# Kernel optimization log

Hardware: AMD Instinct MI355X
Metric: run time of the kernel (lower is better)

The kernel has to match this reference:

```python
import jax, jax.numpy as jnp
import numpy as np

V = 64                 # |Sigma|
IN_DIM = V + 2         # Sigma + '(' + ')'
OUT_DIM = V + 1        # Sigma + <del>/<end>
H = 512
B = 256
SX = 34                # max proto length 32 + 2 boundaries
SY = 34
BIG_NEG = -1000000000.0


def _one_hot_seq(key, S, batch):
    # '(' at pos 0, L random symbols, ')' at pos L+1, zero padding after
    kl, ks = jax.random.split(key)
    lengths = jax.random.randint(kl, (batch,), 4, S - 1)        # L in [4, S-2]
    syms = jax.random.randint(ks, (S, batch), 0, V)
    pos = jnp.arange(S)[:, None]
    tok = jnp.where(pos == 0, V, jnp.where(pos == lengths[None, :] + 1, V + 1, syms))
    oh = jax.nn.one_hot(tok, IN_DIM, dtype=jnp.float32)
    valid = (pos <= lengths[None, :] + 1).astype(jnp.float32)
    return oh * valid[:, :, None]


def setup_inputs() -> dict:
    key = jax.random.key(0)
    ks = jax.random.split(key, 14)

    def p(k, shape, scale):
        return jax.random.uniform(k, shape, jnp.float32, -scale, scale)

    s = 1.0 / float(np.sqrt(H))
    s2 = 1.0 / float(np.sqrt(2 * H))
    return {
        "sources": _one_hot_seq(ks[0], SX, B),
        "targets": _one_hot_seq(ks[1], SY, B),
        # bidirectional prior LSTM (input IN_DIM -> hidden H, fwd + rev)
        "Wih_f": p(ks[2], (4 * H, IN_DIM), s), "Whh_f": p(ks[3], (4 * H, H), s), "b_f": p(ks[4], (4 * H,), s),
        "Wih_r": p(ks[5], (4 * H, IN_DIM), s), "Whh_r": p(ks[6], (4 * H, H), s), "b_r": p(ks[7], (4 * H,), s),
        # modern LSTM (input IN_DIM -> hidden 2H)
        "Wih_m": p(ks[8], (8 * H, IN_DIM), s2), "Whh_m": p(ks[9], (8 * H, 2 * H), s2), "b_m": p(ks[10], (8 * H,), s2),
        # heads: Linear(2H -> OUT_DIM) + LogSoftmax
        "W_sub": p(ks[11], (OUT_DIM, 2 * H), s2), "b_sub": jnp.zeros((OUT_DIM,), jnp.float32),
        "W_ins": p(ks[12], (OUT_DIM, 2 * H), s2), "b_ins": jnp.zeros((OUT_DIM,), jnp.float32),
    }


def _lstm(x, Wih, Whh, b, hid):
    # torch gate order: i, f, g, o
    bsz = x.shape[1]
    def step(carry, xt):
        h, c = carry
        g = xt @ Wih.T + h @ Whh.T + b
        i, f, gg, o = jnp.split(g, 4, axis=-1)
        c = jax.nn.sigmoid(f) * c + jax.nn.sigmoid(i) * jnp.tanh(gg)
        h = jax.nn.sigmoid(o) * jnp.tanh(c)
        return (h, c), h
    init = (jnp.zeros((bsz, hid), x.dtype), jnp.zeros((bsz, hid), x.dtype))
    _, hs = jax.lax.scan(step, init, x)
    return hs  # [S, B, hid]


def _forward(sources, targets, Wih_f, Whh_f, b_f, Wih_r, Whh_r, b_r,
             Wih_m, Whh_m, b_m, W_sub, b_sub, W_ins, b_ins):
    x_fwd = _lstm(sources, Wih_f, Whh_f, b_f, H)
    x_bwd = _lstm(sources[::-1], Wih_r, Whh_r, b_r, H)[::-1]
    x_emb = jnp.concatenate([x_fwd, x_bwd], axis=-1)   # [SX, B, 2H]
    y_emb = _lstm(targets, Wih_m, Whh_m, b_m, 2 * H)    # [SY, B, 2H]

    # head(x_emb[i] + y_emb[j]) decomposes since Linear is affine
    def pair_logprobs(W, bb):
        lx = jnp.einsum('ibh,oh->ibo', x_emb, W)              # [SX, B, O]
        ly = jnp.einsum('jbh,oh->jbo', y_emb, W) + bb         # [SY, B, O]
        return jax.nn.log_softmax(lx[:, None] + ly[None, :], axis=-1)  # [SX, SY, B, O]

    sub_log = pair_logprobs(W_sub, b_sub)
    ins_log = pair_logprobs(W_ins, b_ins)

    # cell (i, j, b) is computed iff x[i] and y[j] are real (non-padding) one-hots, j <= max_cognat_length
    x_any = sources.sum(-1) > 0                                # [SX, B]
    y_any = targets.sum(-1) > 0                                # [SY, B]
    j_ok = jnp.arange(SY) < SY - 1
    valid = x_any[:, None, :] & (y_any & j_ok[:, None])[None, :, :]   # [SX, SY, B]

    end = jnp.where(valid, ins_log[..., V], BIG_NEG)           # insProbs[V_SIZE]
    dlt = jnp.where(valid, sub_log[..., V], BIG_NEG)           # subProbs[V_SIZE]

    y_next = jnp.pad(targets[1:], ((0, 1), (0, 0), (0, 0)))    # y[j+1], [SY, B, IN_DIM]
    ins_ok = valid & (y_next[..., IN_DIM - 1] == 0)[None]      # not bool(y[j+1, V_SIZE+1])
    ins_val = jnp.einsum('ijbv,jbv->ijb', ins_log[..., :V], y_next[..., :V])
    sub_val = jnp.einsum('ijbv,jbv->ijb', sub_log[..., :V], y_next[..., :V])

    # stacked cached probs: [ins, sub, end, del], each [SX, SY, B]
    return jnp.stack([
        jnp.where(ins_ok, ins_val, BIG_NEG),
        jnp.where(ins_ok, sub_val, BIG_NEG),
        end,
        dlt,
    ])


def reference(sources, targets, Wih_f, Whh_f, b_f, Wih_r, Whh_r, b_r,
              Wih_m, Whh_m, b_m, W_sub, b_sub, W_ins, b_ins):
    return _forward(sources, targets, Wih_f, Whh_f, b_f, Wih_r, Whh_r, b_r,
                    Wih_m, Whh_m, b_m, W_sub, b_sub, W_ins, b_ins)
```

## Files before the change

kernel.cpp:

```cpp
#include <hip/hip_runtime.h>

typedef __attribute__((ext_vector_type(4))) float f32x4;
typedef unsigned char u8;
typedef unsigned long long u64t;

#define BIG_NEG -1000000000.0f

static constexpr int B_  = 256;
static constexpr int SX_ = 34;
static constexpr int SY_ = 34;
static constexpr int IND = 66;
static constexpr int OP_ = 80;

__device__ __forceinline__ f32x4 mfma_fp8(long a, long b, f32x4 c) {
  return __builtin_amdgcn_mfma_f32_16x16x32_fp8_fp8(a, b, c, 0, 0, 0);
}
__device__ __forceinline__ float sigm(float x)  { return 1.0f / (1.0f + __expf(-x)); }
__device__ __forceinline__ float tanhx(float x) { return 2.0f * sigm(2.0f * x) - 1.0f; }
template <bool HI>
__device__ __forceinline__ unsigned pk2(float a, float b, unsigned old) {
  return __builtin_amdgcn_cvt_pk_fp8_f32(a, b, (int)old, HI);
}

__global__ __launch_bounds__(256) void prep_all(
    const float* __restrict__ src, const float* __restrict__ tgt,
    int* __restrict__ tok_x, int* __restrict__ tok_y,
    const float* __restrict__ Wsub, const float* __restrict__ Wins,
    u8* __restrict__ Wcat,
    const float* __restrict__ Wihf, const float* __restrict__ bf,
    const float* __restrict__ Wihr, const float* __restrict__ br,
    const float* __restrict__ Wihm, const float* __restrict__ bm,
    float* __restrict__ Ef, float* __restrict__ Er, float* __restrict__ Em,
    const float* __restrict__ Whf, const float* __restrict__ Whr,
    const float* __restrict__ Whm,
    u8* __restrict__ w8f, u8* __restrict__ w8r, u8* __restrict__ w8m) {
  __shared__ float tile[64 * 67];
  const int blk = blockIdx.x;
  const int tid = threadIdx.x;

  if (blk < 68) {
    int idx = blk * 256 + tid;
    const int half = SX_ * B_;
    const float* base = (idx < half) ? src : tgt;
    int* outp         = (idx < half) ? tok_x : tok_y;
    int k = (idx < half) ? idx : idx - half;
    const float* p = base + (size_t)k * IND;
    int tok = -1;
    for (int v = 0; v < IND; ++v) if (p[v] > 0.5f) tok = v;
    outp[k] = tok;
  } else if (blk < 228) {
    int widx = (blk - 68) * 256 + tid;
    int row = widx >> 8;
    int wc  = widx & 255;
    int srow = row < 80 ? row : row - 80;
    const float* W = row < 80 ? Wsub : Wins;
    float f0 = 0.f, f1 = 0.f, f2 = 0.f, f3 = 0.f;
    if (srow < 65) {
      const float* p = W + (size_t)srow * 1024 + wc * 4;
      f0 = p[0]; f1 = p[1]; f2 = p[2]; f3 = p[3];
    }
    unsigned w = pk2<false>(f0, f1, 0);
    w = pk2<true>(f2, f3, w);
    ((unsigned*)Wcat)[widx] = w;
  } else if (blk < 356) {
    int tb = blk - 228;
    const float* W; const float* bias; float* E; int H4; int n0;
    if (tb < 32)      { W = Wihf; bias = bf; E = Ef; H4 = 2048; n0 = tb * 64; }
    else if (tb < 64) { W = Wihr; bias = br; E = Er; H4 = 2048; n0 = (tb - 32) * 64; }
    else              { W = Wihm; bias = bm; E = Em; H4 = 4096; n0 = (tb - 64) * 64; }
    const float* s2 = W + (size_t)n0 * IND;
    for (int i = tid; i < 64 * IND; i += 256) {
      int n = i / IND, v = i - n * IND;
      tile[n * 67 + v] = s2[i];
    }
    __syncthreads();
    int lane = tid & 63, w2 = tid >> 6;
    float bl = bias[n0 + lane];
    for (int v = w2; v < 67; v += 4) {
      float val = (v < 66 ? tile[lane * 67 + v] : 0.f) + bl;
      E[(size_t)v * H4 + n0 + lane] = val;
    }
  } else {
    const int F4 = 2048 * 512 / 4;
    const int M4 = 4096 * 1024 / 4;
    int i = (blk - 356) * 256 + tid;
    int stride = 3072 * 256;
    for (; i < 2 * F4 + M4; i += stride) {
      const float* s3; unsigned* dst; int k;
      if (i < F4)          { s3 = Whf; dst = (unsigned*)w8f; k = i; }
      else if (i < 2 * F4) { s3 = Whr; dst = (unsigned*)w8r; k = i - F4; }
      else                 { s3 = Whm; dst = (unsigned*)w8m; k = i - 2 * F4; }
      float4 f = ((const float4*)s3)[k];
      unsigned w3 = pk2<false>(f.x, f.y, 0);
      w3 = pk2<true>(f.z, f.w, w3);
      dst[k] = w3;
    }
  }
}

template <int HH>
__device__ __forceinline__ void run_lstm(
    const u8* __restrict__ w8, const float* __restrict__ E,
    bool revr, u8* __restrict__ hall, int b0, int h0,
    u8* __restrict__ alds, u8* __restrict__ hT, const u8* __restrict__ tok_small) {
  const int tid = threadIdx.x;
  const int lane = tid & 63, w = tid >> 6;
  const int lo = lane & 15, q = lane >> 4;
  constexpr int AST = HH + 8;
  constexpr int U8C = HH / 8;
  constexpr int USH = (HH == 1024) ? 7 : 6;
  constexpr int NI  = (32 * U8C) / 256;
  constexpr int NK  = HH / 32;
  const int hh = lo & 7;
  const bool hi = (lo >= 8);
  const int hu_e = h0 + w * 8 + hh;
  const unsigned POI = 0x7F7F7F7Fu;

  long breg0[NK], breg1[NK];
  {
    const u8* brow0 = w8 + (size_t)((lo >> 3) * HH + hu_e) * HH + q * 8;
    const u8* brow1 = w8 + (size_t)((2 + (lo >> 3)) * HH + hu_e) * HH + q * 8;
#pragma unroll
    for (int kk = 0; kk < NK; ++kk) {
      breg0[kk] = *(const long*)(brow0 + kk * 32);
      breg1[kk] = *(const long*)(brow1 + kk * 32);
    }
  }
  float creg[4] = {0.f, 0.f, 0.f, 0.f};

  for (int t = 0; t < 34; ++t) {
    const int tpos = revr ? 33 - t : t;
    const u8* tkp = tok_small + tpos * 32;

    float ev[2][4][2];
#pragma unroll
    for (int mt = 0; mt < 2; ++mt)
#pragma unroll
      for (int rr = 0; rr < 2; ++rr) {
        int r = (hi ? 2 : 0) + rr;
        int v = tkp[mt * 16 + q * 4 + r];
        const float* e = E + (size_t)v * (4 * HH) + hu_e;
        ev[mt][0][rr] = e[0];
        ev[mt][1][rr] = e[HH];
        ev[mt][2][rr] = e[2 * HH];
        ev[mt][3][rr] = e[3 * HH];
      }

    f32x4 acc[2][2];
#pragma unroll
    for (int mt = 0; mt < 2; ++mt) {
      acc[mt][0] = (f32x4){0.f, 0.f, 0.f, 0.f};
      acc[mt][1] = (f32x4){0.f, 0.f, 0.f, 0.f};
    }

    if (t > 0) {
      const u8* hsrc = hall + (size_t)t * (256 * HH);
      u64t tmp[NI];
      int spin = 0;
      for (;;) {
        int bad = 0;
#pragma unroll
        for (int ii = 0; ii < NI; ++ii) {
          int idx = tid + ii * 256;
          tmp[ii] = __hip_atomic_load(
              (const u64t*)(hsrc + (size_t)(b0 + (idx >> USH)) * HH + (idx & (U8C - 1)) * 8),
              __ATOMIC_RELAXED, __HIP_MEMORY_SCOPE_AGENT);
          bad |= ((unsigned)tmp[ii] == POI) | ((unsigned)(tmp[ii] >> 32) == POI);
        }
        if (!__syncthreads_or(bad)) break;
        if (++spin > (1 << 15)) break;
      }
#pragma unroll
      for (int ii = 0; ii < NI; ++ii) {
        int idx = tid + ii * 256;
        *(u64t*)&alds[(idx >> USH) * AST + (idx & (U8C - 1)) * 8] = tmp[ii];
      }
      __syncthreads();

      const u8* a0p = alds + lo * AST + q * 8;
      const u8* a1p = alds + (16 + lo) * AST + q * 8;
#pragma unroll
      for (int kk = 0; kk < NK; ++kk) {
        long a0 = *(const long*)(a0p + kk * 32);
        long a1 = *(const long*)(a1p + kk * 32);
        acc[0][0] = mfma_fp8(a0, breg0[kk], acc[0][0]);
        acc[0][1] = mfma_fp8(a0, breg1[kk], acc[0][1]);
        acc[1][0] = mfma_fp8(a1, breg0[kk], acc[1][0]);
        acc[1][1] = mfma_fp8(a1, breg1[kk], acc[1][1]);
      }
    }

#pragma unroll
    for (int mt = 0; mt < 2; ++mt) {
      f32x4 t0 = acc[mt][0], t1 = acc[mt][1];
      f32x4 p0, p1;
#pragma unroll
      for (int c2 = 0; c2 < 4; ++c2) {
        p0[c2] = __shfl_xor(t0[c2], 8, 64);
        p1[c2] = __shfl_xor(t1[c2], 8, 64);
      }
#pragma unroll
      for (int rr = 0; rr < 2; ++rr) {
        int r = (hi ? 2 : 0) + rr;
        float iv = (hi ? p0[r] : t0[r]) + ev[mt][0][rr];
        float fv = (hi ? t0[r] : p0[r]) + ev[mt][1][rr];
        float gv = (hi ? p1[r] : t1[r]) + ev[mt][2][rr];
        float ov = (hi ? t1[r] : p1[r]) + ev[mt][3][rr];
        int m = mt * 16 + q * 4 + r;
        float cold = creg[mt * 2 + rr];
        float cn = sigm(fv) * cold + sigm(iv) * tanhx(gv);
        float hn = sigm(ov) * tanhx(cn);
        creg[mt * 2 + rr] = cn;
        hT[m * 32 + w * 8 + hh] = (u8)(pk2<false>(hn, hn, 0) & 0xffu);
      }
    }
    __syncthreads();

    {
      int m = tid >> 3, cc = tid & 7;
      unsigned val = *(const unsigned*)&hT[m * 32 + cc * 4];
      u8* hdst = hall + (size_t)(t + 1) * (256 * HH);
      __hip_atomic_store((unsigned*)(hdst + (size_t)(b0 + m) * HH + h0 + cc * 4),
                         val, __ATOMIC_RELAXED, __HIP_MEMORY_SCOPE_AGENT);
    }
  }
}

__global__ __launch_bounds__(256, 2) void lstm_persist(
    const int* __restrict__ tok_x, const int* __restrict__ tok_y,
    const float* __restrict__ E_f, const u8* __restrict__ w8_f,
    const float* __restrict__ E_r, const u8* __restrict__ w8_r,
    const float* __restrict__ E_m, const u8* __restrict__ w8_m,
    u8* __restrict__ fwd_all, u8* __restrict__ rev_all, u8* __restrict__ y_all) {
  __shared__ u8 alds[32 * 1032] __attribute__((aligned(16)));
  __shared__ u8 hT[32 * 32] __attribute__((aligned(16)));
  __shared__ u8 tok_small[34 * 32];

  const int b = blockIdx.x;
  int role, c, s;
  if (b < 256)      { role = 2; c = b >> 5; s = b & 31; }
  else if (b < 384) { int l = b - 256; role = 0; c = l >> 4; s = l & 15; }
  else              { int l = b - 384; role = 1; c = l >> 4; s = l & 15; }

  const float* E  = role == 0 ? E_f  : role == 1 ? E_r  : E_m;
  const u8*    w8 = role == 0 ? w8_f : role == 1 ? w8_r : w8_m;
  u8* hall        = role == 0 ? fwd_all : role == 1 ? rev_all : y_all;
  const int* tokg = (role == 2) ? tok_y : tok_x;
  const int b0 = c * 32;
  const int h0 = s * 32;

  for (int i = threadIdx.x; i < 34 * 32; i += 256) {
    int t2 = i >> 5, m = i & 31;
    int tk = tokg[t2 * 256 + b0 + m];
    tok_small[i] = (u8)(tk < 0 ? 66 : tk);
  }
  __syncthreads();

  if (role == 2)
    run_lstm<1024>(w8, E, false, hall, b0, h0, alds, hT, tok_small);
  else
    run_lstm<512>(w8, E, role == 1, hall, b0, h0, alds, hT, tok_small);
}

__global__ __launch_bounds__(256, 1) void head_kernel(
    const u8* __restrict__ fwd_all, const u8* __restrict__ rev_all,
    const u8* __restrict__ y_all, const u8* __restrict__ Wcat,
    const float* __restrict__ b_sub, const float* __restrict__ b_ins,
    float* __restrict__ lx_sub, float* __restrict__ lx_ins,
    float* __restrict__ ly_sub, float* __restrict__ ly_ins) {
  __shared__ u8 wq[160 * 264];
  const int lane = threadIdx.x & 63, wave = threadIdx.x >> 6;
  const int lo = lane & 15, q = lane >> 4;
  int blk = blockIdx.x;
  bool yside = (blk >= 136);
  int mb = yside ? blk - 136 : blk;
  int ij = mb >> 2;
  int bbase = (mb & 3) * 64;

  f32x4 acc[10];
#pragma unroll
  for (int nn = 0; nn < 10; ++nn) acc[nn] = (f32x4){0.f,0.f,0.f,0.f};

  for (int qk = 0; qk < 4; ++qk) {
    long aA[8];
    {
      int row = bbase + wave * 16 + lo;
      const u8* ab;
      if (yside)
        ab = y_all + ((size_t)(ij + 1) * 256 + row) * 1024 + qk * 256 + q * 8;
      else if (qk < 2)
        ab = fwd_all + ((size_t)(ij + 1) * 256 + row) * 512 + qk * 256 + q * 8;
      else
        ab = rev_all + ((size_t)(34 - ij) * 256 + row) * 512 + (qk - 2) * 256 + q * 8;
#pragma unroll
      for (int ki = 0; ki < 8; ++ki) aA[ki] = *(const long*)(ab + ki * 32);
    }

    for (int c8 = threadIdx.x; c8 < 160 * 32; c8 += 256) {
      int row = c8 >> 5, col = (c8 & 31) << 3;
      *(long*)&wq[row * 264 + col] =
          *(const long*)&Wcat[(size_t)row * 1024 + qk * 256 + col];
    }
    __syncthreads();

#pragma unroll
    for (int ki = 0; ki < 8; ++ki) {
#pragma unroll
      for (int nn = 0; nn < 10; ++nn) {
        long bf = *(const long*)&wq[(nn * 16 + lo) * 264 + ki * 32 + q * 8];
        acc[nn] = mfma_fp8(aA[ki], bf, acc[nn]);
      }
    }
    __syncthreads();
  }

#pragma unroll
  for (int nn = 0; nn < 10; ++nn) {
    bool is_sub = (nn < 5);
    int n = (is_sub ? nn : nn - 5) * 16 + lo;
    float bias = 0.0f;
    if (yside && n < 65) bias = is_sub ? b_sub[n] : b_ins[n];
    float* dst = yside ? (is_sub ? ly_sub : ly_ins) : (is_sub ? lx_sub : lx_ins);
#pragma unroll
    for (int r = 0; r < 4; ++r) {
      int b = bbase + wave * 16 + q * 4 + r;
      dst[((size_t)ij * 256 + b) * OP_ + n] = acc[nn][r] + bias;
    }
  }
}

__device__ __forceinline__ void lse_one(const float4* __restrict__ X,
                                        const float* __restrict__ py, int sym,
                                        float& logZ, float& v64, float& vs) {
  float v[68];
  const float4* py4 = (const float4*)py;
#pragma unroll
  for (int q = 0; q < 17; ++q) {
    float4 yb = py4[q];
    v[4 * q + 0] = X[q].x + yb.x;
    v[4 * q + 1] = X[q].y + yb.y;
    v[4 * q + 2] = X[q].z + yb.z;
    v[4 * q + 3] = X[q].w + yb.w;
  }
  float m = v[0];
#pragma unroll
  for (int o = 1; o < 65; ++o) m = fmaxf(m, v[o]);
  float s = 0.0f, vsl = 0.0f;
#pragma unroll
  for (int o = 0; o < 65; ++o) {
    s += __expf(v[o] - m);
    if (o < 64) vsl = (o == sym) ? v[o] : vsl;
  }
  logZ = m + __logf(s);
  v64 = v[64];
  vs = vsl;
}

__global__ __launch_bounds__(256, 1) void pair_kernel(
    const int* __restrict__ tok_x, const int* __restrict__ tok_y,
    const float* __restrict__ lx_sub, const float* __restrict__ lx_ins,
    const float* __restrict__ ly_sub, const float* __restrict__ ly_ins,
    float* __restrict__ out) {
  const int hsel = blockIdx.x >= 136;
  const int rem = hsel ? blockIdx.x - 136 : blockIdx.x;
  const int i = rem >> 2;
  const int bc = rem & 3;
  const int jq = threadIdx.x >> 6;
  const int bl = threadIdx.x & 63;
  const int b = bc * 64 + bl;
  const size_t CH = (size_t)SX_ * SY_ * B_;
  const float* lx = hsel ? lx_ins : lx_sub;
  const float* ly = hsel ? ly_ins : ly_sub;
  float* outA = out + (hsel ? 0 : CH);
  float* outB = out + (hsel ? 2 * CH : 3 * CH);

  float4 X[17];
  {
    const float4* ps = (const float4*)(lx + ((size_t)i * 256 + b) * OP_);
#pragma unroll
    for (int q = 0; q < 17; ++q) X[q] = ps[q];
  }
  int tx = tok_x[i * 256 + b];

  for (int j = jq; j < 34; j += 4) {
    size_t obase = ((size_t)i * SY_ + j) * 256 + b;
    bool dead = (j == SY_ - 1) || (tx < 0);
    if (!dead) {
      int ty = tok_y[j * 256 + b];
      if (ty < 0) dead = true;
    }
    if (dead) {
      outA[obase] = BIG_NEG;
      outB[obase] = BIG_NEG;
      continue;
    }
    int tn = tok_y[(j + 1) * 256 + b];
    bool ins_ok = (tn != 65);
    int sym = (tn >= 0 && tn < 64) ? tn : -1;

    float logZ, v64, vs;
    lse_one(X, ly + ((size_t)j * 256 + b) * OP_, sym, logZ, v64, vs);
    float valB = v64 - logZ;
    float valA = (sym >= 0) ? (vs - logZ) : 0.0f;
    outA[obase] = ins_ok ? valA : BIG_NEG;
    outB[obase] = valB;
  }
}

extern "C" void kernel_launch(void* const* d_in, const int* in_sizes, int n_in,
                              void* d_out, int out_size, void* d_ws, size_t ws_size,
                              hipStream_t stream) {
  const float* sources = (const float*)d_in[0];
  const float* targets = (const float*)d_in[1];
  const float* Wih_f = (const float*)d_in[2];
  const float* Whh_f = (const float*)d_in[3];
  const float* b_f   = (const float*)d_in[4];
  const float* Wih_r = (const float*)d_in[5];
  const float* Whh_r = (const float*)d_in[6];
  const float* b_r   = (const float*)d_in[7];
  const float* Wih_m = (const float*)d_in[8];
  const float* Whh_m = (const float*)d_in[9];
  const float* b_m   = (const float*)d_in[10];
  const float* W_sub = (const float*)d_in[11];
  const float* b_sub = (const float*)d_in[12];
  const float* W_ins = (const float*)d_in[13];
  const float* b_ins = (const float*)d_in[14];
  float* out = (float*)d_out;

  char* w = (char*)d_ws;
  constexpr size_t TOK_SZ  = (size_t)SX_ * B_ * 4;
  constexpr size_t WCAT_SZ = (size_t)160 * 1024;
  constexpr size_t W8F_SZ  = (size_t)2048 * 512;
  constexpr size_t W8M_SZ  = (size_t)4096 * 1024;
  constexpr size_t EF_SZ   = (size_t)67 * 2048 * 4;
  constexpr size_t EM_SZ   = (size_t)67 * 4096 * 4;
  constexpr size_t LX_SZ   = (size_t)SX_ * B_ * OP_ * 4;
  constexpr size_t HF_SZ   = (size_t)35 * B_ * 512;
  constexpr size_t HM_SZ   = (size_t)35 * B_ * 1024;

  size_t off = 0;
  int*  tok_x   = (int*)(w + off);  off += TOK_SZ;
  int*  tok_y   = (int*)(w + off);  off += TOK_SZ;
  off = (off + 255) & ~(size_t)255;
  u8*   Wcat    = (u8*)(w + off);   off += WCAT_SZ;
  u8*   w8_f    = (u8*)(w + off);   off += W8F_SZ;
  u8*   w8_r    = (u8*)(w + off);   off += W8F_SZ;
  u8*   w8_m    = (u8*)(w + off);   off += W8M_SZ;
  float* E_f    = (float*)(w + off); off += EF_SZ;
  float* E_r    = (float*)(w + off); off += EF_SZ;
  float* E_m    = (float*)(w + off); off += EM_SZ;
  float* lx_sub = (float*)(w + off); off += LX_SZ;
  float* lx_ins = (float*)(w + off); off += LX_SZ;
  float* ly_sub = (float*)(w + off); off += LX_SZ;
  float* ly_ins = (float*)(w + off); off += LX_SZ;
  u8* fwd_all   = (u8*)(w + off);   off += HF_SZ;
  u8* rev_all   = (u8*)(w + off);   off += HF_SZ;
  u8* y_all     = (u8*)(w + off);   off += HM_SZ;
  (void)ws_size; (void)in_sizes; (void)n_in; (void)out_size;

  (void)hipMemsetAsync(fwd_all, 0x7F, HF_SZ * 2 + HM_SZ, stream);

  prep_all<<<3428, 256, 0, stream>>>(
      sources, targets, tok_x, tok_y,
      W_sub, W_ins, Wcat,
      Wih_f, b_f, Wih_r, b_r, Wih_m, b_m, E_f, E_r, E_m,
      Whh_f, Whh_r, Whh_m, w8_f, w8_r, w8_m);

  lstm_persist<<<512, 256, 0, stream>>>(
      tok_x, tok_y,
      E_f, w8_f,
      E_r, w8_r,
      E_m, w8_m,
      fwd_all, rev_all, y_all);

  head_kernel<<<272, 256, 0, stream>>>(fwd_all, rev_all, y_all, Wcat,
                                       b_sub, b_ins, lx_sub, lx_ins, ly_sub, ly_ins);

  pair_kernel<<<272, 256, 0, stream>>>(tok_x, tok_y, lx_sub, lx_ins,
                                       ly_sub, ly_ins, out);
}
```

Measured before the change: 398.5 us.

## Use per-block step flags and split modern LSTM across twice as many blocks

Replaces poison-value polling of the hidden-state buffers with per-block step counters. Consumers spin on the producer flags with sleep and then read the hidden state once. The modern 1024-wide LSTM is repartitioned into 16-unit slices with lane shuffles to gather gates, so the grid grows to 768 blocks at 3 per CU. This also drops the large 0x7F memset and cuts redundant re-reads while waiting. The cost is more blocks to synchronise, each waiting on 64 flags, and a dependency on all blocks being co-resident.

```diff
diff --git a/kernel.cpp b/kernel.cpp
--- a/kernel.cpp
+++ b/kernel.cpp
@@ -20,6 +20,11 @@
 template <bool HI>
 __device__ __forceinline__ unsigned pk2(float a, float b, unsigned old) {
   return __builtin_amdgcn_cvt_pk_fp8_f32(a, b, (int)old, HI);
+}
+__device__ __forceinline__ float rsel(f32x4 a, int j) {
+  float lo = (j & 1) ? a[1] : a[0];
+  float hi = (j & 1) ? a[3] : a[2];
+  return (j & 2) ? hi : lo;
 }
 
 __global__ __launch_bounds__(256) void prep_all(
@@ -98,10 +103,12 @@
   }
 }
 
-template <int HH>
-__device__ __forceinline__ void run_lstm(
+
+template <int HH, int NS>
+__device__ __forceinline__ void run_lstm32(
     const u8* __restrict__ w8, const float* __restrict__ E,
     bool revr, u8* __restrict__ hall, int b0, int h0,
+    unsigned* __restrict__ flags, int dom0, int myid,
     u8* __restrict__ alds, u8* __restrict__ hT, const u8* __restrict__ tok_small) {
   const int tid = threadIdx.x;
   const int lane = tid & 63, w = tid >> 6;
@@ -114,7 +121,6 @@
   const int hh = lo & 7;
   const bool hi = (lo >= 8);
   const int hu_e = h0 + w * 8 + hh;
-  const unsigned POI = 0x7F7F7F7Fu;
 
   long breg0[NK], breg1[NK];
   {
@@ -154,21 +160,27 @@
     }
 
     if (t > 0) {
+      if (tid < NS) {
+        const unsigned tgt = (unsigned)t;
+        int spin = 0;
+        for (;;) {
+          unsigned v = __hip_atomic_load(&flags[(dom0 + tid) * 32],
+                                         __ATOMIC_RELAXED, __HIP_MEMORY_SCOPE_AGENT);
+          if (__ballot(v < tgt) == 0) break;
+          __builtin_amdgcn_s_sleep(1);
+          if (++spin > (1 << 17)) break;
+        }
+      }
+      __syncthreads();
+
       const u8* hsrc = hall + (size_t)t * (256 * HH);
       u64t tmp[NI];
-      int spin = 0;
-      for (;;) {
-        int bad = 0;
-#pragma unroll
-        for (int ii = 0; ii < NI; ++ii) {
-          int idx = tid + ii * 256;
-          tmp[ii] = __hip_atomic_load(
-              (const u64t*)(hsrc + (size_t)(b0 + (idx >> USH)) * HH + (idx & (U8C - 1)) * 8),
-              __ATOMIC_RELAXED, __HIP_MEMORY_SCOPE_AGENT);
-          bad |= ((unsigned)tmp[ii] == POI) | ((unsigned)(tmp[ii] >> 32) == POI);
-        }
-        if (!__syncthreads_or(bad)) break;
-        if (++spin > (1 << 15)) break;
+#pragma unroll
+      for (int ii = 0; ii < NI; ++ii) {
+        int idx = tid + ii * 256;
+        tmp[ii] = __hip_atomic_load(
+            (const u64t*)(hsrc + (size_t)(b0 + (idx >> USH)) * HH + (idx & (U8C - 1)) * 8),
+            __ATOMIC_RELAXED, __HIP_MEMORY_SCOPE_AGENT);
       }
 #pragma unroll
       for (int ii = 0; ii < NI; ++ii) {
@@ -223,31 +235,162 @@
       __hip_atomic_store((unsigned*)(hdst + (size_t)(b0 + m) * HH + h0 + cc * 4),
                          val, __ATOMIC_RELAXED, __HIP_MEMORY_SCOPE_AGENT);
     }
-  }
-}
-
-__global__ __launch_bounds__(256, 2) void lstm_persist(
+    if (t < 33) {
+      __asm__ volatile("s_waitcnt vmcnt(0)" ::: "memory");
+      __syncthreads();
+      if (tid == 0)
+        __hip_atomic_store(&flags[(dom0 + myid) * 32], (unsigned)(t + 1),
+                           __ATOMIC_RELAXED, __HIP_MEMORY_SCOPE_AGENT);
+    }
+  }
+}
+
+template <int HH, int NS>
+__device__ __forceinline__ void run_lstm16(
+    const u8* __restrict__ w8, const float* __restrict__ E,
+    u8* __restrict__ hall, int b0, int h0,
+    unsigned* __restrict__ flags, int dom0, int myid,
+    u8* __restrict__ alds, u8* __restrict__ hT, const u8* __restrict__ tok_small) {
+  const int tid = threadIdx.x;
+  const int lane = tid & 63, w = tid >> 6;
+  const int lo = lane & 15, q = lane >> 4;
+  constexpr int AST = HH + 8;
+  constexpr int U8C = HH / 8;
+  constexpr int USH = 7;
+  constexpr int NI  = (32 * U8C) / 256;
+  constexpr int NK  = HH / 32;
+  const int g = lo & 3;
+  const int u = lo >> 2;
+  const int hu = h0 + w * 4 + u;
+
+  long breg[NK];
+  {
+    const u8* brow = w8 + (size_t)(g * HH + hu) * HH + q * 8;
+#pragma unroll
+    for (int kk = 0; kk < NK; ++kk) breg[kk] = *(const long*)(brow + kk * 32);
+  }
+  float creg[2] = {0.f, 0.f};
+
+  for (int t = 0; t < 34; ++t) {
+    const u8* tkp = tok_small + t * 32;
+
+    float ev[2][4];
+#pragma unroll
+    for (int mt = 0; mt < 2; ++mt) {
+      int v = tkp[mt * 16 + q * 4 + g];
+      const float* e = E + (size_t)v * (4 * HH) + hu;
+      ev[mt][0] = e[0]; ev[mt][1] = e[HH]; ev[mt][2] = e[2 * HH]; ev[mt][3] = e[3 * HH];
+    }
+
+    f32x4 acc[2];
+    acc[0] = (f32x4){0.f, 0.f, 0.f, 0.f};
+    acc[1] = (f32x4){0.f, 0.f, 0.f, 0.f};
+
+    if (t > 0) {
+      if (tid < NS) {
+        const unsigned tgt = (unsigned)t;
+        int spin = 0;
+        for (;;) {
+          unsigned v = __hip_atomic_load(&flags[(dom0 + tid) * 32],
+                                         __ATOMIC_RELAXED, __HIP_MEMORY_SCOPE_AGENT);
+          if (__ballot(v < tgt) == 0) break;
+          __builtin_amdgcn_s_sleep(1);
+          if (++spin > (1 << 17)) break;
+        }
+      }
+      __syncthreads();
+
+      const u8* hsrc = hall + (size_t)t * (256 * HH);
+      u64t tmp[NI];
+#pragma unroll
+      for (int ii = 0; ii < NI; ++ii) {
+        int idx = tid + ii * 256;
+        tmp[ii] = __hip_atomic_load(
+            (const u64t*)(hsrc + (size_t)(b0 + (idx >> USH)) * HH + (idx & (U8C - 1)) * 8),
+            __ATOMIC_RELAXED, __HIP_MEMORY_SCOPE_AGENT);
+      }
+#pragma unroll
+      for (int ii = 0; ii < NI; ++ii) {
+        int idx = tid + ii * 256;
+        *(u64t*)&alds[(idx >> USH) * AST + (idx & (U8C - 1)) * 8] = tmp[ii];
+      }
+      __syncthreads();
+
+      const u8* a0p = alds + lo * AST + q * 8;
+      const u8* a1p = alds + (16 + lo) * AST + q * 8;
+#pragma unroll
+      for (int kk = 0; kk < NK; ++kk) {
+        long a0 = *(const long*)(a0p + kk * 32);
+        long a1 = *(const long*)(a1p + kk * 32);
+        acc[0] = mfma_fp8(a0, breg[kk], acc[0]);
+        acc[1] = mfma_fp8(a1, breg[kk], acc[1]);
+      }
+    }
+
+#pragma unroll
+    for (int mt = 0; mt < 2; ++mt) {
+      f32x4 a = acc[mt];
+      float own = rsel(a, g);
+      float y1  = __shfl_xor(rsel(a, g ^ 1), 1, 64);
+      float y2  = __shfl_xor(rsel(a, g ^ 2), 2, 64);
+      float y3  = __shfl_xor(rsel(a, g ^ 3), 3, 64);
+      float iv = (g == 0) ? own : (g == 1) ? y1 : (g == 2) ? y2 : y3;
+      float fv = (g == 0) ? y1 : (g == 1) ? own : (g == 2) ? y3 : y2;
+      float gv = (g == 0) ? y2 : (g == 1) ? y3 : (g == 2) ? own : y1;
+      float ov = (g == 0) ? y3 : (g == 1) ? y2 : (g == 2) ? y1 : own;
+      iv += ev[mt][0]; fv += ev[mt][1]; gv += ev[mt][2]; ov += ev[mt][3];
+      int m = mt * 16 + q * 4 + g;
+      float cold = creg[mt];
+      float cn = sigm(fv) * cold + sigm(iv) * tanhx(gv);
+      float hn = sigm(ov) * tanhx(cn);
+      creg[mt] = cn;
+      hT[m * 16 + w * 4 + u] = (u8)(pk2<false>(hn, hn, 0) & 0xffu);
+    }
+    __syncthreads();
+
+    if (tid < 128) {
+      int m = tid >> 2, cc = tid & 3;
+      unsigned val = *(const unsigned*)&hT[m * 16 + cc * 4];
+      u8* hdst = hall + (size_t)(t + 1) * (256 * HH);
+      __hip_atomic_store((unsigned*)(hdst + (size_t)(b0 + m) * HH + h0 + cc * 4),
+                         val, __ATOMIC_RELAXED, __HIP_MEMORY_SCOPE_AGENT);
+    }
+    if (t < 33) {
+      __asm__ volatile("s_waitcnt vmcnt(0)" ::: "memory");
+      __syncthreads();
+      if (tid == 0)
+        __hip_atomic_store(&flags[(dom0 + myid) * 32], (unsigned)(t + 1),
+                           __ATOMIC_RELAXED, __HIP_MEMORY_SCOPE_AGENT);
+    }
+  }
+}
+
+__global__ __launch_bounds__(256, 3) void lstm_persist(
     const int* __restrict__ tok_x, const int* __restrict__ tok_y,
     const float* __restrict__ E_f, const u8* __restrict__ w8_f,
     const float* __restrict__ E_r, const u8* __restrict__ w8_r,
     const float* __restrict__ E_m, const u8* __restrict__ w8_m,
-    u8* __restrict__ fwd_all, u8* __restrict__ rev_all, u8* __restrict__ y_all) {
+    u8* __restrict__ fwd_all, u8* __restrict__ rev_all, u8* __restrict__ y_all,
+    unsigned* __restrict__ flags) {
   __shared__ u8 alds[32 * 1032] __attribute__((aligned(16)));
   __shared__ u8 hT[32 * 32] __attribute__((aligned(16)));
   __shared__ u8 tok_small[34 * 32];
 
   const int b = blockIdx.x;
   int role, c, s;
-  if (b < 256)      { role = 2; c = b >> 5; s = b & 31; }
-  else if (b < 384) { int l = b - 256; role = 0; c = l >> 4; s = l & 15; }
-  else              { int l = b - 384; role = 1; c = l >> 4; s = l & 15; }
+  if (b < 512)      { role = 2; c = b >> 6; s = b & 63; }
+  else if (b < 640) { int l = b - 512; role = 0; c = l >> 4; s = l & 15; }
+  else              { int l = b - 640; role = 1; c = l >> 4; s = l & 15; }
 
   const float* E  = role == 0 ? E_f  : role == 1 ? E_r  : E_m;
   const u8*    w8 = role == 0 ? w8_f : role == 1 ? w8_r : w8_m;
   u8* hall        = role == 0 ? fwd_all : role == 1 ? rev_all : y_all;
   const int* tokg = (role == 2) ? tok_y : tok_x;
   const int b0 = c * 32;
-  const int h0 = s * 32;
+  int dom0, h0;
+  if (role == 2)      { dom0 = c * 64;       h0 = s * 16; }
+  else if (role == 0) { dom0 = 512 + c * 16; h0 = s * 32; }
+  else                { dom0 = 640 + c * 16; h0 = s * 32; }
 
   for (int i = threadIdx.x; i < 34 * 32; i += 256) {
     int t2 = i >> 5, m = i & 31;
@@ -257,9 +400,10 @@
   __syncthreads();
 
   if (role == 2)
-    run_lstm<1024>(w8, E, false, hall, b0, h0, alds, hT, tok_small);
+    run_lstm16<1024, 64>(w8, E, hall, b0, h0, flags, dom0, s, alds, hT, tok_small);
   else
-    run_lstm<512>(w8, E, role == 1, hall, b0, h0, alds, hT, tok_small);
+    run_lstm32<512, 16>(w8, E, role == 1, hall, b0, h0, flags, dom0, s, alds, hT,
+                        tok_small);
 }
 
 __global__ __launch_bounds__(256, 1) void head_kernel(
@@ -428,6 +572,7 @@
   float* out = (float*)d_out;
 
   char* w = (char*)d_ws;
+  constexpr size_t FLAG_SZ = 768 * 32 * 4;
   constexpr size_t TOK_SZ  = (size_t)SX_ * B_ * 4;
   constexpr size_t WCAT_SZ = (size_t)160 * 1024;
   constexpr size_t W8F_SZ  = (size_t)2048 * 512;
@@ -439,6 +584,7 @@
   constexpr size_t HM_SZ   = (size_t)35 * B_ * 1024;
 
   size_t off = 0;
+  unsigned* flags = (unsigned*)(w + off); off += FLAG_SZ;
   int*  tok_x   = (int*)(w + off);  off += TOK_SZ;
   int*  tok_y   = (int*)(w + off);  off += TOK_SZ;
   off = (off + 255) & ~(size_t)255;
@@ -458,7 +604,7 @@
   u8* y_all     = (u8*)(w + off);   off += HM_SZ;
   (void)ws_size; (void)in_sizes; (void)n_in; (void)out_size;
 
-  (void)hipMemsetAsync(fwd_all, 0x7F, HF_SZ * 2 + HM_SZ, stream);
+  (void)hipMemsetAsync(flags, 0, FLAG_SZ, stream);
 
   prep_all<<<3428, 256, 0, stream>>>(
       sources, targets, tok_x, tok_y,
@@ -466,12 +612,12 @@
       Wih_f, b_f, Wih_r, b_r, Wih_m, b_m, E_f, E_r, E_m,
       Whh_f, Whh_r, Whh_m, w8_f, w8_r, w8_m);
 
-  lstm_persist<<<512, 256, 0, stream>>>(
+  lstm_persist<<<768, 256, 0, stream>>>(
       tok_x, tok_y,
       E_f, w8_f,
       E_r, w8_r,
       E_m, w8_m,
-      fwd_all, rev_all, y_all);
+      fwd_all, rev_all, y_all, flags);
 
   head_kernel<<<272, 256, 0, stream>>>(fwd_all, rev_all, y_all, Wcat,
                                        b_sub, b_ins, lx_sub, lx_ins, ly_sub, ly_ins);
```

Measured after the change: 338.2 us. 1.18x faster.
